# Optimization experiments

Measured on AMD Instinct MI355X. Metric: run time of the kernel, lower is better.

## Reference

```python
import jax, jax.numpy as jnp
import numpy as np

B, S, H, F, E = 2, 2048, 1024, 4096, 8  # batch, seq, hidden, ffn, num_experts


def setup_inputs() -> dict:
    key = jax.random.key(0)
    ks = jax.random.split(key, 4)
    x = jax.random.normal(ks[0], (B, S, H), dtype=jnp.float32)
    w_router = jax.random.normal(ks[1], (H, E), dtype=jnp.float32) * 0.02
    w1 = jax.random.normal(ks[2], (E, H, F), dtype=jnp.float32) * 0.02
    b1 = jnp.zeros((E, F), dtype=jnp.float32)
    w2 = jax.random.normal(ks[3], (E, F, H), dtype=jnp.float32) * 0.02
    b2 = jnp.zeros((E, H), dtype=jnp.float32)
    return {"x": x, "w_router": w_router, "w1": w1, "b1": b1, "w2": w2, "b2": b2}


def reference(x, w_router, w1, b1, w2, b2):
    """Top-1 MoE layer: route -> per-expert FFN -> weighted combine.

    Faithful to ExpertParallelWrapper._process_moe_layer on a single group:
    router picks one expert per token with a routing weight; tokens are
    dispatched to experts (here expressed as a static mask over the fixed
    expert set), processed by the expert FFN, and scatter-combined back
    weighted by the routing probability.
    """
    Bs, Ss, Hs = x.shape
    n_experts = w1.shape[0]
    # Router: per-token logits -> softmax -> top-1 expert + weight
    logits = jnp.einsum('bsh,he->bse', x, w_router)          # [B,S,E]
    probs = jax.nn.softmax(logits, axis=-1)
    sel = jnp.argmax(probs, axis=-1)                          # [B,S] selected expert
    wgt = jnp.take_along_axis(probs, sel[..., None], axis=-1)[..., 0]  # [B,S]

    xt = x.reshape(-1, Hs)        # [T,H] flat tokens
    sel_t = sel.reshape(-1)       # [T]
    wgt_t = wgt.reshape(-1)       # [T]

    out = jnp.zeros_like(xt)
    # Static loop over the small fixed expert set (dispatch/combine via mask).
    for e in range(n_experts):
        h = jax.nn.relu(xt @ w1[e] + b1[e])   # [T,F]
        y = h @ w2[e] + b2[e]                 # [T,H]
        m = (sel_t == e).astype(xt.dtype) * wgt_t
        out = out + m[:, None] * y
    return out.reshape(Bs, Ss, Hs)
```

## Files before the change

### kernel.cpp

```cpp
#include <hip/hip_runtime.h>
#include <math.h>

#define T_TOK 4096
#define H_DIM 1024
#define F_DIM 4096
#define E_NUM 8
#define BK 32

typedef __attribute__((ext_vector_type(8))) short bhalf8_t;
typedef __attribute__((ext_vector_type(4))) float f32x4_t;

__device__ __forceinline__ unsigned short f2bf(float f) {
  unsigned int u = __float_as_uint(f);
  return (unsigned short)((u + 0x7fffu + ((u >> 16) & 1u)) >> 16);
}

__device__ __forceinline__ void gload16(const void* g, void* l) {
  __builtin_amdgcn_global_load_lds(
      (const __attribute__((address_space(1))) unsigned int*)g,
      (__attribute__((address_space(3))) unsigned int*)l, 16, 0, 0);
}

__global__ void k_init(int* counts) {
  if (threadIdx.x < E_NUM) counts[threadIdx.x] = 0;
}

__global__ void k_router(const float* __restrict__ x, const float* __restrict__ wr,
                         int* __restrict__ sel, float* __restrict__ wgt,
                         int* __restrict__ counts) {
  const int t = blockIdx.x;
  const int lane = threadIdx.x;
  const float* xr = x + (size_t)t * H_DIM;
  double acc[E_NUM] = {0, 0, 0, 0, 0, 0, 0, 0};
  for (int h = lane; h < H_DIM; h += 64) {
    const double xv = (double)xr[h];
    const float* w = wr + (size_t)h * E_NUM;
#pragma unroll
    for (int e = 0; e < E_NUM; ++e) acc[e] += xv * (double)w[e];
  }
#pragma unroll
  for (int e = 0; e < E_NUM; ++e) {
#pragma unroll
    for (int off = 32; off > 0; off >>= 1) acc[e] += __shfl_down(acc[e], off, 64);
  }
  if (lane == 0) {
    double m = acc[0];
    int a = 0;
#pragma unroll
    for (int e = 1; e < E_NUM; ++e)
      if (acc[e] > m) { m = acc[e]; a = e; }
    double s = 0.0;
#pragma unroll
    for (int e = 0; e < E_NUM; ++e) s += exp(acc[e] - m);
    sel[t] = a;
    wgt[t] = (float)(1.0 / s);
    atomicAdd(&counts[a], 1);
  }
}

__global__ void k_prefix(const int* __restrict__ counts, int* __restrict__ offs,
                         int* __restrict__ cursors) {
  if (threadIdx.x == 0 && blockIdx.x == 0) {
    int s = 0;
    for (int e = 0; e < E_NUM; ++e) {
      offs[e] = s;
      cursors[e] = s;
      s += counts[e];
    }
    offs[E_NUM] = s;
  }
}

__global__ void k_scatter(const float* __restrict__ x, const int* __restrict__ sel,
                          const float* __restrict__ wgt, int* __restrict__ cursors,
                          int* __restrict__ s2t, float* __restrict__ wgtS,
                          unsigned short* __restrict__ Xs) {
  const int t = blockIdx.x;
  __shared__ int sslot;
  if (threadIdx.x == 0) {
    const int slot = atomicAdd(&cursors[sel[t]], 1);
    sslot = slot;
    s2t[slot] = t;
    wgtS[slot] = wgt[t];
  }
  __syncthreads();
  const int slot = sslot;
  const float4 v = reinterpret_cast<const float4*>(x + (size_t)t * H_DIM)[threadIdx.x];
  ushort4 o;
  o.x = f2bf(v.x); o.y = f2bf(v.y); o.z = f2bf(v.z); o.w = f2bf(v.w);
  reinterpret_cast<ushort4*>(Xs + (size_t)slot * H_DIM)[threadIdx.x] = o;
}

__global__ void k_transpose(const float* __restrict__ in, unsigned short* __restrict__ out,
                            int K, int N) {
  const int e = blockIdx.z;
  const int n0 = blockIdx.x * 64;
  const int k0 = blockIdx.y * 64;
  __shared__ float tile[64][65];
  const float* src = in + (size_t)e * K * N;
  unsigned short* dst = out + (size_t)e * N * K;
  const int tx = threadIdx.x & 63;
  const int ty = threadIdx.x >> 6;
#pragma unroll
  for (int i = 0; i < 64; i += 4)
    tile[ty + i][tx] = src[(size_t)(k0 + ty + i) * N + (n0 + tx)];
  __syncthreads();
#pragma unroll
  for (int i = 0; i < 64; i += 4)
    dst[(size_t)(n0 + ty + i) * K + (k0 + tx)] = f2bf(tile[tx][ty + i]);
}

__global__ __launch_bounds__(256) void k_ffn1(const unsigned short* __restrict__ Xs,
                                              const unsigned short* __restrict__ Wt,
                                              const float* __restrict__ b1,
                                              unsigned short* __restrict__ Hws,
                                              const int* __restrict__ offs) {
  const int e = blockIdx.z;
  const int off = offs[e];
  const int cnt = offs[e + 1] - off;
  const int m0 = blockIdx.y * 128;
  if (m0 >= cnt) return;
  const int n0 = blockIdx.x * 128;
  const int msize = cnt - m0;

  __shared__ short lA[128 * BK];
  __shared__ short lB[128 * BK];

  const int tid = threadIdx.x;
  const int lane = tid & 63;
  const int wv = tid >> 6;
  const int wm = (wv >> 1) * 64;
  const int wn = (wv & 1) * 64;

  const int sRow = lane >> 2;
  const int sCol = (lane & 3) * 8;

  const unsigned short* Abase = Xs + (size_t)off * H_DIM;
  const unsigned short* Bbase = Wt + (size_t)e * F_DIM * H_DIM + (size_t)n0 * H_DIM;

  f32x4_t acc[4][4];
#pragma unroll
  for (int i = 0; i < 4; ++i)
#pragma unroll
    for (int j = 0; j < 4; ++j) acc[i][j] = (f32x4_t){0.f, 0.f, 0.f, 0.f};

  for (int k0 = 0; k0 < H_DIM; k0 += BK) {
    __syncthreads();
#pragma unroll
    for (int i = 0; i < 2; ++i) {
      const int g = wv * 2 + i;
      const int row = g * 16 + sRow;
      int ar = row;
      if (ar >= msize) ar = 0;
      gload16(Abase + (size_t)(m0 + ar) * H_DIM + k0 + sCol, &lA[g * 16 * BK]);
      gload16(Bbase + (size_t)row * H_DIM + k0 + sCol, &lB[g * 16 * BK]);
    }
    __syncthreads();

    const int q = lane >> 4;
    const int r16 = lane & 15;
    bhalf8_t af[4], bf[4];
#pragma unroll
    for (int mi = 0; mi < 4; ++mi)
      af[mi] = *reinterpret_cast<const bhalf8_t*>(&lA[(wm + mi * 16 + r16) * BK + q * 8]);
#pragma unroll
    for (int ni = 0; ni < 4; ++ni)
      bf[ni] = *reinterpret_cast<const bhalf8_t*>(&lB[(wn + ni * 16 + r16) * BK + q * 8]);
#pragma unroll
    for (int mi = 0; mi < 4; ++mi)
#pragma unroll
      for (int ni = 0; ni < 4; ++ni)
        acc[mi][ni] = __builtin_amdgcn_mfma_f32_16x16x32_bf16(af[mi], bf[ni], acc[mi][ni], 0, 0, 0);
  }

  const int q = lane >> 4;
  const int c = lane & 15;
#pragma unroll
  for (int ni = 0; ni < 4; ++ni) {
    const int col = n0 + wn + ni * 16 + c;
    const float bias = b1[e * F_DIM + col];
#pragma unroll
    for (int mi = 0; mi < 4; ++mi) {
      const int rbase = wm + mi * 16 + q * 4;
#pragma unroll
      for (int r = 0; r < 4; ++r) {
        const int row = rbase + r;
        if (row < msize) {
          float v = acc[mi][ni][r] + bias;
          v = fmaxf(v, 0.0f);
          Hws[(size_t)(off + m0 + row) * F_DIM + col] = f2bf(v);
        }
      }
    }
  }
}

__global__ __launch_bounds__(256) void k_ffn2(const unsigned short* __restrict__ Hws,
                                              const unsigned short* __restrict__ Wt,
                                              const float* __restrict__ b2,
                                              const int* __restrict__ offs,
                                              const int* __restrict__ s2t,
                                              const float* __restrict__ wgtS,
                                              float* __restrict__ out) {
  const int e = blockIdx.z;
  const int off = offs[e];
  const int cnt = offs[e + 1] - off;
  const int m0 = blockIdx.y * 128;
  if (m0 >= cnt) return;
  const int n0 = blockIdx.x * 128;
  const int msize = cnt - m0;

  __shared__ short lA[128 * BK];
  __shared__ short lB[128 * BK];

  const int tid = threadIdx.x;
  const int lane = tid & 63;
  const int wv = tid >> 6;
  const int wm = (wv >> 1) * 64;
  const int wn = (wv & 1) * 64;

  const int sRow = lane >> 2;
  const int sCol = (lane & 3) * 8;

  const unsigned short* Abase = Hws + (size_t)off * F_DIM;
  const unsigned short* Bbase = Wt + (size_t)e * H_DIM * F_DIM + (size_t)n0 * F_DIM;

  f32x4_t acc[4][4];
#pragma unroll
  for (int i = 0; i < 4; ++i)
#pragma unroll
    for (int j = 0; j < 4; ++j) acc[i][j] = (f32x4_t){0.f, 0.f, 0.f, 0.f};

  for (int k0 = 0; k0 < F_DIM; k0 += BK) {
    __syncthreads();
#pragma unroll
    for (int i = 0; i < 2; ++i) {
      const int g = wv * 2 + i;
      const int row = g * 16 + sRow;
      int ar = row;
      if (ar >= msize) ar = 0;
      gload16(Abase + (size_t)(m0 + ar) * F_DIM + k0 + sCol, &lA[g * 16 * BK]);
      gload16(Bbase + (size_t)row * F_DIM + k0 + sCol, &lB[g * 16 * BK]);
    }
    __syncthreads();

    const int q = lane >> 4;
    const int r16 = lane & 15;
    bhalf8_t af[4], bf[4];
#pragma unroll
    for (int mi = 0; mi < 4; ++mi)
      af[mi] = *reinterpret_cast<const bhalf8_t*>(&lA[(wm + mi * 16 + r16) * BK + q * 8]);
#pragma unroll
    for (int ni = 0; ni < 4; ++ni)
      bf[ni] = *reinterpret_cast<const bhalf8_t*>(&lB[(wn + ni * 16 + r16) * BK + q * 8]);
#pragma unroll
    for (int mi = 0; mi < 4; ++mi)
#pragma unroll
      for (int ni = 0; ni < 4; ++ni)
        acc[mi][ni] = __builtin_amdgcn_mfma_f32_16x16x32_bf16(af[mi], bf[ni], acc[mi][ni], 0, 0, 0);
  }

  const int q = lane >> 4;
  const int c = lane & 15;
#pragma unroll
  for (int mi = 0; mi < 4; ++mi) {
    const int rbase = wm + mi * 16 + q * 4;
#pragma unroll
    for (int r = 0; r < 4; ++r) {
      const int row = rbase + r;
      if (row >= msize) continue;
      const int srow = off + m0 + row;
      const int tok = s2t[srow];
      const float w = wgtS[srow];
      float* orow = out + (size_t)tok * H_DIM;
#pragma unroll
      for (int ni = 0; ni < 4; ++ni) {
        const int col = n0 + wn + ni * 16 + c;
        orow[col] = w * (acc[mi][ni][r] + b2[e * H_DIM + col]);
      }
    }
  }
}

extern "C" void kernel_launch(void* const* d_in, const int* in_sizes, int n_in,
                              void* d_out, int out_size, void* d_ws, size_t ws_size,
                              hipStream_t stream) {
  const float* x  = (const float*)d_in[0];
  const float* wr = (const float*)d_in[1];
  const float* w1 = (const float*)d_in[2];
  const float* b1 = (const float*)d_in[3];
  const float* w2 = (const float*)d_in[4];
  const float* b2 = (const float*)d_in[5];
  float* out = (float*)d_out;

  char* ws = (char*)d_ws;
  unsigned short* WT  = (unsigned short*)(ws);
  unsigned short* XS  = (unsigned short*)(ws + 67108864);
  unsigned short* HWS = (unsigned short*)(ws + 67108864 + 8388608);
  char* ctrl = ws + 67108864 + 8388608 + 33554432;
  int*   sel     = (int*)(ctrl);
  int*   s2t     = (int*)(ctrl + 16384);
  float* wgt     = (float*)(ctrl + 32768);
  float* wgtS    = (float*)(ctrl + 49152);
  int*   counts  = (int*)(ctrl + 65536);
  int*   offs    = (int*)(ctrl + 65536 + 64);
  int*   cursors = (int*)(ctrl + 65536 + 128);

  k_init<<<1, 64, 0, stream>>>(counts);
  k_router<<<T_TOK, 64, 0, stream>>>(x, wr, sel, wgt, counts);
  k_prefix<<<1, 1, 0, stream>>>(counts, offs, cursors);
  k_scatter<<<T_TOK, 256, 0, stream>>>(x, sel, wgt, cursors, s2t, wgtS, XS);

  k_transpose<<<dim3(F_DIM / 64, H_DIM / 64, E_NUM), 256, 0, stream>>>(w1, WT, H_DIM, F_DIM);
  k_ffn1<<<dim3(F_DIM / 128, T_TOK / 128, E_NUM), 256, 0, stream>>>(XS, WT, b1, HWS, offs);

  k_transpose<<<dim3(H_DIM / 64, F_DIM / 64, E_NUM), 256, 0, stream>>>(w2, WT, F_DIM, H_DIM);
  k_ffn2<<<dim3(H_DIM / 128, T_TOK / 128, E_NUM), 256, 0, stream>>>(HWS, WT, b2, offs, s2t, wgtS, out);
}
```

Measured before the change: 581.4 us.

## Split-K ffn2 with atomics, swizzle LDS tiles, vectorize transpose stores

The second expert GEMM is split four ways along F and partial results are combined with atomicAdd into an output that a new kernel zeros first. This raises block count where few tokens per expert leave the GPU underfilled. Both GEMMs also XOR-swizzle the LDS column chunk to cut bank conflicts on fragment reads. The transpose now writes bf16 pairs as ushort2 instead of single shorts. The trade-offs are atomic traffic, an extra zeroing pass, and summation order that varies between runs.

```diff
diff --git a/kernel.cpp b/kernel.cpp
--- a/kernel.cpp
+++ b/kernel.cpp
@@ -6,6 +6,7 @@
 #define F_DIM 4096
 #define E_NUM 8
 #define BK 32
+#define KSPLIT 4
 
 typedef __attribute__((ext_vector_type(8))) short bhalf8_t;
 typedef __attribute__((ext_vector_type(4))) float f32x4_t;
@@ -23,6 +24,10 @@
 
 __global__ void k_init(int* counts) {
   if (threadIdx.x < E_NUM) counts[threadIdx.x] = 0;
+}
+
+__global__ void k_zero(float4* out) {
+  out[(size_t)blockIdx.x * 256 + threadIdx.x] = (float4){0.f, 0.f, 0.f, 0.f};
 }
 
 __global__ void k_router(const float* __restrict__ x, const float* __restrict__ wr,
@@ -105,9 +110,16 @@
   for (int i = 0; i < 64; i += 4)
     tile[ty + i][tx] = src[(size_t)(k0 + ty + i) * N + (n0 + tx)];
   __syncthreads();
-#pragma unroll
-  for (int i = 0; i < 64; i += 4)
-    dst[(size_t)(n0 + ty + i) * K + (k0 + tx)] = f2bf(tile[tx][ty + i]);
+  const int kx = (threadIdx.x & 31) * 2;
+  const int ny = threadIdx.x >> 5;
+#pragma unroll
+  for (int i = 0; i < 64; i += 8) {
+    const int n = ny + i;
+    ushort2 o;
+    o.x = f2bf(tile[kx][n]);
+    o.y = f2bf(tile[kx + 1][n]);
+    *reinterpret_cast<ushort2*>(&dst[(size_t)(n0 + n) * K + (k0 + kx)]) = o;
+  }
 }
 
 __global__ __launch_bounds__(256) void k_ffn1(const unsigned short* __restrict__ Xs,
@@ -133,7 +145,8 @@
   const int wn = (wv & 1) * 64;
 
   const int sRow = lane >> 2;
-  const int sCol = (lane & 3) * 8;
+  const int cc = lane & 3;
+  const int sCol = (cc ^ ((sRow >> 1) & 3)) * 8;
 
   const unsigned short* Abase = Xs + (size_t)off * H_DIM;
   const unsigned short* Bbase = Wt + (size_t)e * F_DIM * H_DIM + (size_t)n0 * H_DIM;
@@ -159,13 +172,14 @@
 
     const int q = lane >> 4;
     const int r16 = lane & 15;
+    const int sw = ((r16 >> 1) & 3);
     bhalf8_t af[4], bf[4];
 #pragma unroll
     for (int mi = 0; mi < 4; ++mi)
-      af[mi] = *reinterpret_cast<const bhalf8_t*>(&lA[(wm + mi * 16 + r16) * BK + q * 8]);
+      af[mi] = *reinterpret_cast<const bhalf8_t*>(&lA[(wm + mi * 16 + r16) * BK + (q ^ sw) * 8]);
 #pragma unroll
     for (int ni = 0; ni < 4; ++ni)
-      bf[ni] = *reinterpret_cast<const bhalf8_t*>(&lB[(wn + ni * 16 + r16) * BK + q * 8]);
+      bf[ni] = *reinterpret_cast<const bhalf8_t*>(&lB[(wn + ni * 16 + r16) * BK + (q ^ sw) * 8]);
 #pragma unroll
     for (int mi = 0; mi < 4; ++mi)
 #pragma unroll
@@ -202,13 +216,16 @@
                                               const int* __restrict__ s2t,
                                               const float* __restrict__ wgtS,
                                               float* __restrict__ out) {
-  const int e = blockIdx.z;
+  const int e = blockIdx.z >> 2;
+  const int ks = blockIdx.z & 3;
   const int off = offs[e];
   const int cnt = offs[e + 1] - off;
   const int m0 = blockIdx.y * 128;
   if (m0 >= cnt) return;
   const int n0 = blockIdx.x * 128;
   const int msize = cnt - m0;
+  const int kbeg = ks * (F_DIM / KSPLIT);
+  const int kend = kbeg + (F_DIM / KSPLIT);
 
   __shared__ short lA[128 * BK];
   __shared__ short lB[128 * BK];
@@ -220,7 +237,8 @@
   const int wn = (wv & 1) * 64;
 
   const int sRow = lane >> 2;
-  const int sCol = (lane & 3) * 8;
+  const int cc = lane & 3;
+  const int sCol = (cc ^ ((sRow >> 1) & 3)) * 8;
 
   const unsigned short* Abase = Hws + (size_t)off * F_DIM;
   const unsigned short* Bbase = Wt + (size_t)e * H_DIM * F_DIM + (size_t)n0 * F_DIM;
@@ -231,7 +249,7 @@
 #pragma unroll
     for (int j = 0; j < 4; ++j) acc[i][j] = (f32x4_t){0.f, 0.f, 0.f, 0.f};
 
-  for (int k0 = 0; k0 < F_DIM; k0 += BK) {
+  for (int k0 = kbeg; k0 < kend; k0 += BK) {
     __syncthreads();
 #pragma unroll
     for (int i = 0; i < 2; ++i) {
@@ -246,13 +264,14 @@
 
     const int q = lane >> 4;
     const int r16 = lane & 15;
+    const int sw = ((r16 >> 1) & 3);
     bhalf8_t af[4], bf[4];
 #pragma unroll
     for (int mi = 0; mi < 4; ++mi)
-      af[mi] = *reinterpret_cast<const bhalf8_t*>(&lA[(wm + mi * 16 + r16) * BK + q * 8]);
+      af[mi] = *reinterpret_cast<const bhalf8_t*>(&lA[(wm + mi * 16 + r16) * BK + (q ^ sw) * 8]);
 #pragma unroll
     for (int ni = 0; ni < 4; ++ni)
-      bf[ni] = *reinterpret_cast<const bhalf8_t*>(&lB[(wn + ni * 16 + r16) * BK + q * 8]);
+      bf[ni] = *reinterpret_cast<const bhalf8_t*>(&lB[(wn + ni * 16 + r16) * BK + (q ^ sw) * 8]);
 #pragma unroll
     for (int mi = 0; mi < 4; ++mi)
 #pragma unroll
@@ -276,7 +295,9 @@
 #pragma unroll
       for (int ni = 0; ni < 4; ++ni) {
         const int col = n0 + wn + ni * 16 + c;
-        orow[col] = w * (acc[mi][ni][r] + b2[e * H_DIM + col]);
+        float v = acc[mi][ni][r];
+        if (ks == 0) v += b2[e * H_DIM + col];
+        atomicAdd(&orow[col], w * v);
       }
     }
   }
@@ -307,6 +328,7 @@
   int*   cursors = (int*)(ctrl + 65536 + 128);
 
   k_init<<<1, 64, 0, stream>>>(counts);
+  k_zero<<<T_TOK * H_DIM / (256 * 4), 256, 0, stream>>>((float4*)out);
   k_router<<<T_TOK, 64, 0, stream>>>(x, wr, sel, wgt, counts);
   k_prefix<<<1, 1, 0, stream>>>(counts, offs, cursors);
   k_scatter<<<T_TOK, 256, 0, stream>>>(x, sel, wgt, cursors, s2t, wgtS, XS);
@@ -315,5 +337,5 @@
   k_ffn1<<<dim3(F_DIM / 128, T_TOK / 128, E_NUM), 256, 0, stream>>>(XS, WT, b1, HWS, offs);
 
   k_transpose<<<dim3(H_DIM / 64, F_DIM / 64, E_NUM), 256, 0, stream>>>(w2, WT, F_DIM, H_DIM);
-  k_ffn2<<<dim3(H_DIM / 128, T_TOK / 128, E_NUM), 256, 0, stream>>>(HWS, WT, b2, offs, s2t, wgtS, out);
-}
+  k_ffn2<<<dim3(H_DIM / 128, T_TOK / 128, E_NUM * KSPLIT), 256, 0, stream>>>(HWS, WT, b2, offs, s2t, wgtS, out);
+}
```

New measurement: 607.5 us. 4.5% more time.
